# Performance work log

Hardware: AMD Instinct MI355X
Metric: run time of the kernel (lower is better)

Reference implementation:

```python
import jax, jax.numpy as jnp
import numpy as np

N_EMBED = 1024
NUM_EXPERTS = 8
TOP_K = 2
D_FF = 4 * N_EMBED
B, S = 4, 2048


def setup_inputs() -> dict:
    key = jax.random.key(0)
    ks = jax.random.split(key, 8)
    s = 0.02
    return {
        "x": jax.random.normal(ks[0], (B, S, N_EMBED), jnp.float32),
        "noise": jax.random.normal(ks[1], (B, S, NUM_EXPERTS), jnp.float32),
        "w_route": jax.random.normal(ks[2], (N_EMBED, NUM_EXPERTS), jnp.float32) * s,
        "b_route": jnp.zeros((NUM_EXPERTS,), jnp.float32),
        "w_noise": jax.random.normal(ks[3], (N_EMBED, NUM_EXPERTS), jnp.float32) * s,
        "b_noise": jnp.zeros((NUM_EXPERTS,), jnp.float32),
        "w1": jax.random.normal(ks[4], (NUM_EXPERTS, N_EMBED, D_FF), jnp.float32) * s,
        "b1": jnp.zeros((NUM_EXPERTS, D_FF), jnp.float32),
        "w2": jax.random.normal(ks[5], (NUM_EXPERTS, D_FF, N_EMBED), jnp.float32) * s,
        "b2": jnp.zeros((NUM_EXPERTS, N_EMBED), jnp.float32),
    }


def reference(x, noise, w_route, b_route, w_noise, b_noise, w1, b1, w2, b2):
    # NoisyTopkRouter: logits + N(0,1)*softplus(noise_logits), top-k, softmax
    # over a sparse (-inf filled) logit matrix -> gates are exactly 0 for
    # non-selected experts.
    logits = x @ w_route + b_route                                   # [B,S,E]
    noise_logits = x @ w_noise + b_noise                             # [B,S,E]
    noisy = logits + noise * jax.nn.softplus(noise_logits)           # [B,S,E]
    _, topi = jax.lax.top_k(noisy, TOP_K)                            # [B,S,k]
    sel = jax.nn.one_hot(topi, NUM_EXPERTS, dtype=bool).any(-2)      # [B,S,E]
    sparse_logits = jnp.where(sel, noisy, -jnp.inf)
    gates = jax.nn.softmax(sparse_logits, axis=-1)                   # [B,S,E]

    T = x.shape[0] * x.shape[1]
    xf = x.reshape(T, N_EMBED)                                       # [T,d]
    gf = gates.reshape(T, NUM_EXPERTS)                               # [T,E]

    # Dense per-expert MLP weighted by gates; gate==0 for unselected tokens,
    # so this matches the masked gather/scatter of the original exactly.
    out = jnp.zeros_like(xf)
    for e in range(NUM_EXPERTS):
        h = jax.nn.relu(xf @ w1[e] + b1[e])                          # [T,4d]
        y = h @ w2[e] + b2[e]                                        # [T,d]
        out = out + y * gf[:, e:e + 1]
    return out.reshape(x.shape)
```

## Files before the change

### kernel.cpp

```cpp
#include <hip/hip_runtime.h>

typedef __bf16 bf16_t;
typedef __bf16 bf16x8 __attribute__((ext_vector_type(8)));
typedef __bf16 bf16x4 __attribute__((ext_vector_type(4)));
typedef float  f32x4  __attribute__((ext_vector_type(4)));

#define T_TOK 8192
#define DIM   1024
#define DFF   4096
#define NEXP  8

__device__ __forceinline__ void gll16(const void* g, void* l) {
    __builtin_amdgcn_global_load_lds(
        (const __attribute__((address_space(1))) char*)g,
        (__attribute__((address_space(3))) char*)l, 16, 0, 0);
}

__global__ __launch_bounds__(256) void transpose_cvt_kernel(
    const float* __restrict__ src, bf16_t* __restrict__ dst, int R, int C) {
    __shared__ float t[64][65];
    int e = blockIdx.z;
    src += (size_t)e * R * C;
    dst += (size_t)e * R * C;
    int r0 = blockIdx.y * 64, c0 = blockIdx.x * 64;
    int tid = threadIdx.x;
    {
        int cg = tid & 15, r = tid >> 4;
#pragma unroll
        for (int i = 0; i < 4; ++i) {
            int rr = r + i * 16;
            float4 v = *(const float4*)&src[(size_t)(r0 + rr) * C + c0 + cg * 4];
            t[rr][cg * 4 + 0] = v.x; t[rr][cg * 4 + 1] = v.y;
            t[rr][cg * 4 + 2] = v.z; t[rr][cg * 4 + 3] = v.w;
        }
    }
    __syncthreads();
    {
        int rr = tid & 7, c = tid >> 3;
#pragma unroll
        for (int i = 0; i < 2; ++i) {
            int cc = c + i * 32;
            bf16x8 o;
#pragma unroll
            for (int j = 0; j < 8; ++j) o[j] = (bf16_t)t[rr * 8 + j][cc];
            *(bf16x8*)&dst[(size_t)(c0 + cc) * R + r0 + rr * 8] = o;
        }
    }
}

__global__ __launch_bounds__(256) void router_kernel(
    const float* __restrict__ x, const float* __restrict__ noise,
    const float* __restrict__ w_route, const float* __restrict__ b_route,
    const float* __restrict__ w_noise, const float* __restrict__ b_noise,
    int* __restrict__ counts, int* __restrict__ lists, float* __restrict__ gate_tok)
{
    int wave = threadIdx.x >> 6;
    int lane = threadIdx.x & 63;
    int t = blockIdx.x * 4 + wave;
    if (t >= T_TOK) return;

    const float* xr = x + (size_t)t * DIM;
    double aR[NEXP], aN[NEXP];
#pragma unroll
    for (int e = 0; e < NEXP; ++e) { aR[e] = 0.0; aN[e] = 0.0; }

#pragma unroll 4
    for (int i = 0; i < 16; ++i) {
        int k = lane + i * 64;
        double xv = (double)xr[k];
        const float4* wr4 = (const float4*)(w_route + (size_t)k * 8);
        const float4* wn4 = (const float4*)(w_noise + (size_t)k * 8);
        float4 r0 = wr4[0], r1 = wr4[1];
        float4 n0 = wn4[0], n1 = wn4[1];
        aR[0] += xv * (double)r0.x; aR[1] += xv * (double)r0.y;
        aR[2] += xv * (double)r0.z; aR[3] += xv * (double)r0.w;
        aR[4] += xv * (double)r1.x; aR[5] += xv * (double)r1.y;
        aR[6] += xv * (double)r1.z; aR[7] += xv * (double)r1.w;
        aN[0] += xv * (double)n0.x; aN[1] += xv * (double)n0.y;
        aN[2] += xv * (double)n0.z; aN[3] += xv * (double)n0.w;
        aN[4] += xv * (double)n1.x; aN[5] += xv * (double)n1.y;
        aN[6] += xv * (double)n1.z; aN[7] += xv * (double)n1.w;
    }
#pragma unroll
    for (int e = 0; e < NEXP; ++e) {
        for (int s = 1; s < 64; s <<= 1) {
            aR[e] += __shfl_xor(aR[e], s);
            aN[e] += __shfl_xor(aN[e], s);
        }
    }
    if (lane == 0) {
        double nv[NEXP];
#pragma unroll
        for (int e = 0; e < NEXP; ++e) {
            double lg = aR[e] + (double)b_route[e];
            double nl = aN[e] + (double)b_noise[e];
            double sp = (nl > 30.0) ? nl : log1p(exp(nl));
            nv[e] = lg + (double)noise[(size_t)t * 8 + e] * sp;
        }
        int i1 = 0;
#pragma unroll
        for (int e = 1; e < NEXP; ++e) if (nv[e] > nv[i1]) i1 = e;
        int i2 = (i1 == 0) ? 1 : 0;
#pragma unroll
        for (int e = 0; e < NEXP; ++e) if (e != i1 && nv[e] > nv[i2]) i2 = e;
        double m = nv[i1];
        double e2 = exp(nv[i2] - m);
        double s = 1.0 + e2;
        gate_tok[2 * t + 0] = (float)(1.0 / s);
        gate_tok[2 * t + 1] = (float)(e2 / s);
        int p1 = atomicAdd(&counts[i1], 1);
        lists[i1 * T_TOK + p1] = 2 * t + 0;
        int p2 = atomicAdd(&counts[i2], 1);
        lists[i2 * T_TOK + p2] = 2 * t + 1;
    }
}

__global__ void prefix_kernel(const int* __restrict__ counts, int* __restrict__ bases) {
    if (threadIdx.x == 0 && blockIdx.x == 0) {
        int s = 0;
#pragma unroll
        for (int e = 0; e < NEXP; ++e) { bases[e] = s; s += counts[e]; }
    }
}

__global__ __launch_bounds__(256) void pack_a_kernel(
    const float* __restrict__ x, const int* __restrict__ bases,
    const int* __restrict__ lists, bf16_t* __restrict__ Ap, int* __restrict__ inv)
{
    int wave = threadIdx.x >> 6, lane = threadIdx.x & 63;
    int p = blockIdx.x * 4 + wave;
    int e = 0;
#pragma unroll
    for (int i = 1; i < NEXP; ++i) e += (p >= bases[i]);
    int pos = p - bases[e];
    int entry = lists[e * T_TOK + pos];
    if (lane == 0) inv[entry] = p;
    const float4* src = (const float4*)(x + (size_t)(entry >> 1) * DIM);
    bf16x4* dst = (bf16x4*)(Ap + (size_t)p * DIM);
#pragma unroll
    for (int j = 0; j < 4; ++j) {
        float4 v = src[lane + j * 64];
        bf16x4 o;
        o[0] = (bf16_t)v.x; o[1] = (bf16_t)v.y; o[2] = (bf16_t)v.z; o[3] = (bf16_t)v.w;
        dst[lane + j * 64] = o;
    }
}

template<int K, int MODE>
__global__ __launch_bounds__(256) void moe_gemm_kernel(
    const bf16_t* __restrict__ Asrc, const bf16_t* __restrict__ Wt,
    const float* __restrict__ bias,
    const int* __restrict__ counts, const int* __restrict__ bases,
    const int* __restrict__ lists, const float* __restrict__ gate_tok,
    bf16_t* __restrict__ Hout, float* __restrict__ Yp)
{
    constexpr int N = (MODE == 0) ? DFF : DIM;
    constexpr int NT = K / 64;
    constexpr int NY = N / 128;

    int wg = blockIdx.x + 64 * (blockIdx.y + NY * blockIdx.z);
    int e = wg & 7;
    int inner = wg >> 3;
    int xi = inner & 63;
    int yi = inner >> 6;

    int cnt = counts[e];
    int m0 = xi * 128;
    if (m0 >= cnt) return;
    int base = bases[e];
    int n0 = yi * 128;
    const int* list = lists + e * T_TOK;
    const bf16_t* W = Wt + (size_t)e * N * K;

    __shared__ __attribute__((aligned(16))) bf16_t Ah0[128 * 64];
    __shared__ __attribute__((aligned(16))) bf16_t Bh0[128 * 64];
    __shared__ __attribute__((aligned(16))) bf16_t Ah1[128 * 64];
    __shared__ __attribute__((aligned(16))) bf16_t Bh1[128 * 64];

    int tid = threadIdx.x;
    int lane = tid & 63;
    int wave = tid >> 6;
    int wr = wave >> 1, wc = wave & 1;

    int kcs = (((lane & 7) ^ (lane >> 3)) << 3);
    const bf16_t* pA[4];
    const bf16_t* pB[4];
#pragma unroll
    for (int i = 0; i < 4; ++i) {
        int c = wave * 4 + i;
        int r = c * 8 + (lane >> 3);
        int ridx = m0 + r; if (ridx > cnt - 1) ridx = cnt - 1;
        pA[i] = Asrc + (size_t)(base + ridx) * K + kcs;
        pB[i] = W + (size_t)(n0 + r) * K + kcs;
    }

    f32x4 acc[4][4];
#pragma unroll
    for (int m = 0; m < 4; ++m)
#pragma unroll
        for (int n = 0; n < 4; ++n)
            acc[m][n] = (f32x4){0.f, 0.f, 0.f, 0.f};

    int g = lane >> 4, ln15 = lane & 15, ln7 = lane & 7;

#define STAGE(An, Bn, k0) do {                                               \
    _Pragma("unroll") for (int i = 0; i < 4; ++i) {                          \
        int c = wave * 4 + i;                                                \
        gll16(pA[i] + (k0), (An) + c * 512);                                 \
        gll16(pB[i] + (k0), (Bn) + c * 512);                                 \
    } } while (0)

#define COMPUTE(Ab, Bb) do {                                                 \
    _Pragma("unroll") for (int kk = 0; kk < 2; ++kk) {                       \
        bf16x8 a[4], b[4];                                                   \
        int sw = (((kk * 4 + g) ^ ln7) << 3);                                \
        _Pragma("unroll") for (int n = 0; n < 4; ++n)                        \
            b[n] = *(const bf16x8*)((Bb) + (wc * 64 + n * 16 + ln15) * 64 + sw); \
        _Pragma("unroll") for (int m = 0; m < 4; ++m)                        \
            a[m] = *(const bf16x8*)((Ab) + (wr * 64 + m * 16 + ln15) * 64 + sw); \
        __builtin_amdgcn_s_setprio(1);                                       \
        _Pragma("unroll") for (int m = 0; m < 4; ++m)                        \
            _Pragma("unroll") for (int n = 0; n < 4; ++n)                    \
                acc[m][n] = __builtin_amdgcn_mfma_f32_16x16x32_bf16(a[m], b[n], acc[m][n], 0, 0, 0); \
        __builtin_amdgcn_s_setprio(0);                                       \
    } } while (0)

#define FENCE() __builtin_amdgcn_sched_barrier(0)
#define WAITV(n) asm volatile("s_waitcnt vmcnt(" #n ")" ::: "memory")

    STAGE(Ah0, Bh0, 0);

    for (int kt = 0; kt < NT; kt += 2) {
        if (kt + 1 < NT) { STAGE(Ah1, Bh1, (kt + 1) * 64); WAITV(8); }
        else             { WAITV(0); }
        FENCE(); __builtin_amdgcn_s_barrier(); FENCE();
        COMPUTE(Ah0, Bh0);
        FENCE(); __builtin_amdgcn_s_barrier(); FENCE();
        if (kt + 2 < NT) { STAGE(Ah0, Bh0, (kt + 2) * 64); WAITV(8); }
        else             { WAITV(0); }
        FENCE(); __builtin_amdgcn_s_barrier(); FENCE();
        COMPUTE(Ah1, Bh1);
        FENCE(); __builtin_amdgcn_s_barrier(); FENCE();
    }
#undef STAGE
#undef COMPUTE
#undef FENCE
#undef WAITV

    int l4 = lane >> 4;
    float bs[4];
#pragma unroll
    for (int n = 0; n < 4; ++n)
        bs[n] = bias[e * N + n0 + wc * 64 + n * 16 + ln15];
#pragma unroll
    for (int m = 0; m < 4; ++m) {
#pragma unroll
        for (int j = 0; j < 4; ++j) {
            int grow = m0 + wr * 64 + m * 16 + l4 * 4 + j;
            if (grow >= cnt) continue;
            if constexpr (MODE == 0) {
#pragma unroll
                for (int n = 0; n < 4; ++n) {
                    int gcol = n0 + wc * 64 + n * 16 + ln15;
                    float v = acc[m][n][j] + bs[n];
                    Hout[(size_t)(base + grow) * DFF + gcol] = (bf16_t)fmaxf(v, 0.f);
                }
            } else {
                float gt = gate_tok[list[grow]];
#pragma unroll
                for (int n = 0; n < 4; ++n) {
                    int gcol = n0 + wc * 64 + n * 16 + ln15;
                    Yp[(size_t)(base + grow) * DIM + gcol] = gt * (acc[m][n][j] + bs[n]);
                }
            }
        }
    }
}

__global__ __launch_bounds__(256) void combine_kernel(
    const float* __restrict__ Yp, const int* __restrict__ inv,
    float* __restrict__ out)
{
#pragma unroll
    for (int q = 0; q < 2; ++q) {
        int t = blockIdx.x * 2 + q;
        int p0 = inv[2 * t], p1 = inv[2 * t + 1];
        const float4* a = (const float4*)(Yp + (size_t)p0 * DIM);
        const float4* b = (const float4*)(Yp + (size_t)p1 * DIM);
        float4* o = (float4*)(out + (size_t)t * DIM);
        int i = threadIdx.x;
        float4 va = a[i], vb = b[i];
        o[i] = make_float4(va.x + vb.x, va.y + vb.y, va.z + vb.z, va.w + vb.w);
    }
}

extern "C" void kernel_launch(void* const* d_in, const int* in_sizes, int n_in,
                              void* d_out, int out_size, void* d_ws, size_t ws_size,
                              hipStream_t stream) {
    const float* x       = (const float*)d_in[0];
    const float* noise   = (const float*)d_in[1];
    const float* w_route = (const float*)d_in[2];
    const float* b_route = (const float*)d_in[3];
    const float* w_noise = (const float*)d_in[4];
    const float* b_noise = (const float*)d_in[5];
    const float* w1      = (const float*)d_in[6];
    const float* b1      = (const float*)d_in[7];
    const float* w2      = (const float*)d_in[8];
    const float* b2      = (const float*)d_in[9];
    float* out = (float*)d_out;

    char* ws = (char*)d_ws;
    size_t off = 0;
    auto alloc = [&](size_t bytes) {
        off = (off + 255) & ~(size_t)255;
        size_t r = off; off += bytes; return r;
    };
    int*    counts   = (int*)   (ws + alloc(32));
    int*    bases    = (int*)   (ws + alloc(32));
    int*    lists    = (int*)   (ws + alloc((size_t)NEXP * T_TOK * 4));
    float*  gate_tok = (float*) (ws + alloc((size_t)T_TOK * 2 * 4));
    int*    inv      = (int*)   (ws + alloc((size_t)T_TOK * 2 * 4));
    bf16_t* w1t      = (bf16_t*)(ws + alloc((size_t)NEXP * DFF * DIM * 2));
    bf16_t* w2t      = (bf16_t*)(ws + alloc((size_t)NEXP * DIM * DFF * 2));
    bf16_t* Ap       = (bf16_t*)(ws + alloc((size_t)T_TOK * 2 * DIM * 2));
    bf16_t* H        = (bf16_t*)(ws + alloc((size_t)T_TOK * 2 * DFF * 2));
    float*  Yp       = (float*)w1t;
    (void)ws_size; (void)in_sizes; (void)n_in; (void)out_size;

    hipMemsetAsync(counts, 0, 32, stream);

    transpose_cvt_kernel<<<dim3(DFF / 64, DIM / 64, NEXP), 256, 0, stream>>>(w1, w1t, DIM, DFF);
    transpose_cvt_kernel<<<dim3(DIM / 64, DFF / 64, NEXP), 256, 0, stream>>>(w2, w2t, DFF, DIM);

    router_kernel<<<T_TOK / 4, 256, 0, stream>>>(x, noise, w_route, b_route, w_noise, b_noise,
                                                 counts, lists, gate_tok);
    prefix_kernel<<<1, 64, 0, stream>>>(counts, bases);
    pack_a_kernel<<<T_TOK * 2 / 4, 256, 0, stream>>>(x, bases, lists, Ap, inv);

    moe_gemm_kernel<DIM, 0><<<dim3(64, DFF / 128, NEXP), 256, 0, stream>>>(
        Ap, w1t, b1, counts, bases, lists, gate_tok, H, nullptr);
    moe_gemm_kernel<DFF, 1><<<dim3(64, DIM / 128, NEXP), 256, 0, stream>>>(
        H, w2t, b2, counts, bases, lists, gate_tok, nullptr, Yp);

    combine_kernel<<<T_TOK / 2, 256, 0, stream>>>(Yp, inv, out);
}
```

Measured before the change: 780.2 us.

## Enlarge MoE GEMM tile to 256x128 with K-step 32

Changes the grouped expert GEMM tile from 128x128 with a 64-wide K step to 256x128 with a 32-wide K step. Each wave now computes 128x64 outputs with 8x4 MFMA accumulators, which raises arithmetic intensity per LDS byte and per global load. The LDS swizzle, staging layout, wait counts and launch grid are reworked to match. In exchange it uses more accumulator registers, which may reduce occupancy. It also needs twice as many K iterations with barriers, and padding waste grows for experts whose token count is not a multiple of 256.

```diff
diff --git a/kernel.cpp b/kernel.cpp
--- a/kernel.cpp
+++ b/kernel.cpp
@@ -155,75 +155,79 @@
     bf16_t* __restrict__ Hout, float* __restrict__ Yp)
 {
     constexpr int N = (MODE == 0) ? DFF : DIM;
-    constexpr int NT = K / 64;
+    constexpr int NT = K / 32;
     constexpr int NY = N / 128;
 
-    int wg = blockIdx.x + 64 * (blockIdx.y + NY * blockIdx.z);
+    int wg = blockIdx.x + 32 * (blockIdx.y + NY * blockIdx.z);
     int e = wg & 7;
     int inner = wg >> 3;
-    int xi = inner & 63;
-    int yi = inner >> 6;
+    int xi = inner & 31;
+    int yi = inner >> 5;
 
     int cnt = counts[e];
-    int m0 = xi * 128;
+    int m0 = xi * 256;
     if (m0 >= cnt) return;
     int base = bases[e];
     int n0 = yi * 128;
     const int* list = lists + e * T_TOK;
     const bf16_t* W = Wt + (size_t)e * N * K;
 
-    __shared__ __attribute__((aligned(16))) bf16_t Ah0[128 * 64];
-    __shared__ __attribute__((aligned(16))) bf16_t Bh0[128 * 64];
-    __shared__ __attribute__((aligned(16))) bf16_t Ah1[128 * 64];
-    __shared__ __attribute__((aligned(16))) bf16_t Bh1[128 * 64];
+    __shared__ __attribute__((aligned(16))) bf16_t Ah0[256 * 32];
+    __shared__ __attribute__((aligned(16))) bf16_t Bh0[128 * 32];
+    __shared__ __attribute__((aligned(16))) bf16_t Ah1[256 * 32];
+    __shared__ __attribute__((aligned(16))) bf16_t Bh1[128 * 32];
 
     int tid = threadIdx.x;
     int lane = tid & 63;
     int wave = tid >> 6;
     int wr = wave >> 1, wc = wave & 1;
 
-    int kcs = (((lane & 7) ^ (lane >> 3)) << 3);
+    int kcs = (((lane & 3) ^ ((lane >> 3) & 3)) << 3);
     const bf16_t* pA[4];
-    const bf16_t* pB[4];
+    const bf16_t* pB[2];
 #pragma unroll
     for (int i = 0; i < 4; ++i) {
         int c = wave * 4 + i;
-        int r = c * 8 + (lane >> 3);
+        int r = c * 16 + (lane >> 2);
         int ridx = m0 + r; if (ridx > cnt - 1) ridx = cnt - 1;
         pA[i] = Asrc + (size_t)(base + ridx) * K + kcs;
+    }
+#pragma unroll
+    for (int i = 0; i < 2; ++i) {
+        int c = wave * 2 + i;
+        int r = c * 16 + (lane >> 2);
         pB[i] = W + (size_t)(n0 + r) * K + kcs;
     }
 
-    f32x4 acc[4][4];
-#pragma unroll
-    for (int m = 0; m < 4; ++m)
+    f32x4 acc[8][4];
+#pragma unroll
+    for (int m = 0; m < 8; ++m)
 #pragma unroll
         for (int n = 0; n < 4; ++n)
             acc[m][n] = (f32x4){0.f, 0.f, 0.f, 0.f};
 
-    int g = lane >> 4, ln15 = lane & 15, ln7 = lane & 7;
+    int g = lane >> 4, ln15 = lane & 15;
+    int sw = ((g ^ ((ln15 >> 1) & 3)) << 3);
 
 #define STAGE(An, Bn, k0) do {                                               \
-    _Pragma("unroll") for (int i = 0; i < 4; ++i) {                          \
-        int c = wave * 4 + i;                                                \
-        gll16(pA[i] + (k0), (An) + c * 512);                                 \
-        gll16(pB[i] + (k0), (Bn) + c * 512);                                 \
-    } } while (0)
+    _Pragma("unroll") for (int i = 0; i < 4; ++i)                            \
+        gll16(pA[i] + (k0), (An) + (wave * 4 + i) * 512);                    \
+    _Pragma("unroll") for (int i = 0; i < 2; ++i)                            \
+        gll16(pB[i] + (k0), (Bn) + (wave * 2 + i) * 512);                    \
+    } while (0)
 
 #define COMPUTE(Ab, Bb) do {                                                 \
-    _Pragma("unroll") for (int kk = 0; kk < 2; ++kk) {                       \
-        bf16x8 a[4], b[4];                                                   \
-        int sw = (((kk * 4 + g) ^ ln7) << 3);                                \
+    bf16x8 b[4];                                                             \
+    _Pragma("unroll") for (int n = 0; n < 4; ++n)                            \
+        b[n] = *(const bf16x8*)((Bb) + (wc * 64 + n * 16 + ln15) * 32 + sw); \
+    __builtin_amdgcn_s_setprio(1);                                           \
+    _Pragma("unroll") for (int m = 0; m < 8; ++m) {                          \
+        bf16x8 a = *(const bf16x8*)((Ab) + (wr * 128 + m * 16 + ln15) * 32 + sw); \
         _Pragma("unroll") for (int n = 0; n < 4; ++n)                        \
-            b[n] = *(const bf16x8*)((Bb) + (wc * 64 + n * 16 + ln15) * 64 + sw); \
-        _Pragma("unroll") for (int m = 0; m < 4; ++m)                        \
-            a[m] = *(const bf16x8*)((Ab) + (wr * 64 + m * 16 + ln15) * 64 + sw); \
-        __builtin_amdgcn_s_setprio(1);                                       \
-        _Pragma("unroll") for (int m = 0; m < 4; ++m)                        \
-            _Pragma("unroll") for (int n = 0; n < 4; ++n)                    \
-                acc[m][n] = __builtin_amdgcn_mfma_f32_16x16x32_bf16(a[m], b[n], acc[m][n], 0, 0, 0); \
-        __builtin_amdgcn_s_setprio(0);                                       \
-    } } while (0)
+            acc[m][n] = __builtin_amdgcn_mfma_f32_16x16x32_bf16(a, b[n], acc[m][n], 0, 0, 0); \
+    }                                                                        \
+    __builtin_amdgcn_s_setprio(0);                                           \
+    } while (0)
 
 #define FENCE() __builtin_amdgcn_sched_barrier(0)
 #define WAITV(n) asm volatile("s_waitcnt vmcnt(" #n ")" ::: "memory")
@@ -231,12 +235,12 @@
     STAGE(Ah0, Bh0, 0);
 
     for (int kt = 0; kt < NT; kt += 2) {
-        if (kt + 1 < NT) { STAGE(Ah1, Bh1, (kt + 1) * 64); WAITV(8); }
+        if (kt + 1 < NT) { STAGE(Ah1, Bh1, (kt + 1) * 32); WAITV(6); }
         else             { WAITV(0); }
         FENCE(); __builtin_amdgcn_s_barrier(); FENCE();
         COMPUTE(Ah0, Bh0);
         FENCE(); __builtin_amdgcn_s_barrier(); FENCE();
-        if (kt + 2 < NT) { STAGE(Ah0, Bh0, (kt + 2) * 64); WAITV(8); }
+        if (kt + 2 < NT) { STAGE(Ah0, Bh0, (kt + 2) * 32); WAITV(6); }
         else             { WAITV(0); }
         FENCE(); __builtin_amdgcn_s_barrier(); FENCE();
         COMPUTE(Ah1, Bh1);
@@ -253,10 +257,10 @@
     for (int n = 0; n < 4; ++n)
         bs[n] = bias[e * N + n0 + wc * 64 + n * 16 + ln15];
 #pragma unroll
-    for (int m = 0; m < 4; ++m) {
+    for (int m = 0; m < 8; ++m) {
 #pragma unroll
         for (int j = 0; j < 4; ++j) {
-            int grow = m0 + wr * 64 + m * 16 + l4 * 4 + j;
+            int grow = m0 + wr * 128 + m * 16 + l4 * 4 + j;
             if (grow >= cnt) continue;
             if constexpr (MODE == 0) {
 #pragma unroll
@@ -337,9 +341,9 @@
     prefix_kernel<<<1, 64, 0, stream>>>(counts, bases);
     pack_a_kernel<<<T_TOK * 2 / 4, 256, 0, stream>>>(x, bases, lists, Ap, inv);
 
-    moe_gemm_kernel<DIM, 0><<<dim3(64, DFF / 128, NEXP), 256, 0, stream>>>(
+    moe_gemm_kernel<DIM, 0><<<dim3(32, DFF / 128, NEXP), 256, 0, stream>>>(
         Ap, w1t, b1, counts, bases, lists, gate_tok, H, nullptr);
-    moe_gemm_kernel<DFF, 1><<<dim3(64, DIM / 128, NEXP), 256, 0, stream>>>(
+    moe_gemm_kernel<DFF, 1><<<dim3(32, DIM / 128, NEXP), 256, 0, stream>>>(
         H, w2t, b2, counts, bases, lists, gate_tok, nullptr, Yp);
 
     combine_kernel<<<T_TOK / 2, 256, 0, stream>>>(Yp, inv, out);
```

Result: slower. 1.025 ms (+31.4%).

## Inline expert prefix sums and restructure GEMM double-buffer to one barrier per tile

Applied to the files above, without the earlier changes.

The single-thread prefix_kernel launch is removed. pack_a and the MoE GEMM kernels now compute expert base offsets themselves from the 8 counts. The GEMM main loop changes from a stage, partial-wait, barrier, compute, barrier sequence to staging the next tile, computing the current one, then a full vmcnt drain and a single barrier. This halves the barriers per K-tile and removes one kernel launch. The cost is that each compute step now waits on the full drain of the prefetch, so less memory latency may be hidden if loads outlast compute.

```diff
diff --git a/kernel.cpp b/kernel.cpp
--- a/kernel.cpp
+++ b/kernel.cpp
@@ -115,24 +115,22 @@
     }
 }
 
-__global__ void prefix_kernel(const int* __restrict__ counts, int* __restrict__ bases) {
-    if (threadIdx.x == 0 && blockIdx.x == 0) {
-        int s = 0;
-#pragma unroll
-        for (int e = 0; e < NEXP; ++e) { bases[e] = s; s += counts[e]; }
-    }
-}
-
 __global__ __launch_bounds__(256) void pack_a_kernel(
-    const float* __restrict__ x, const int* __restrict__ bases,
+    const float* __restrict__ x, const int* __restrict__ counts,
     const int* __restrict__ lists, bf16_t* __restrict__ Ap, int* __restrict__ inv)
 {
     int wave = threadIdx.x >> 6, lane = threadIdx.x & 63;
     int p = blockIdx.x * 4 + wave;
+    int bs[NEXP];
+    {
+        int s = 0;
+#pragma unroll
+        for (int i = 0; i < NEXP; ++i) { bs[i] = s; s += counts[i]; }
+    }
     int e = 0;
 #pragma unroll
-    for (int i = 1; i < NEXP; ++i) e += (p >= bases[i]);
-    int pos = p - bases[e];
+    for (int i = 1; i < NEXP; ++i) e += (p >= bs[i]);
+    int pos = p - bs[e];
     int entry = lists[e * T_TOK + pos];
     if (lane == 0) inv[entry] = p;
     const float4* src = (const float4*)(x + (size_t)(entry >> 1) * DIM);
@@ -150,8 +148,8 @@
 __global__ __launch_bounds__(256) void moe_gemm_kernel(
     const bf16_t* __restrict__ Asrc, const bf16_t* __restrict__ Wt,
     const float* __restrict__ bias,
-    const int* __restrict__ counts, const int* __restrict__ bases,
-    const int* __restrict__ lists, const float* __restrict__ gate_tok,
+    const int* __restrict__ counts, const int* __restrict__ lists,
+    const float* __restrict__ gate_tok,
     bf16_t* __restrict__ Hout, float* __restrict__ Yp)
 {
     constexpr int N = (MODE == 0) ? DFF : DIM;
@@ -164,10 +162,19 @@
     int xi = inner & 63;
     int yi = inner >> 6;
 
-    int cnt = counts[e];
+    int cnt, base;
+    {
+        int s = 0, c = 0;
+#pragma unroll
+        for (int i = 0; i < NEXP; ++i) {
+            int ci = counts[i];
+            if (i == e) { base = s; c = ci; }
+            s += ci;
+        }
+        cnt = c;
+    }
     int m0 = xi * 128;
     if (m0 >= cnt) return;
-    int base = bases[e];
     int n0 = yi * 128;
     const int* list = lists + e * T_TOK;
     const bf16_t* W = Wt + (size_t)e * N * K;
@@ -226,26 +233,25 @@
     } } while (0)
 
 #define FENCE() __builtin_amdgcn_sched_barrier(0)
-#define WAITV(n) asm volatile("s_waitcnt vmcnt(" #n ")" ::: "memory")
+#define DRAIN() asm volatile("s_waitcnt vmcnt(0)" ::: "memory")
+#define BARR()  do { FENCE(); __builtin_amdgcn_s_barrier(); FENCE(); } while (0)
 
     STAGE(Ah0, Bh0, 0);
+    DRAIN(); BARR();
 
     for (int kt = 0; kt < NT; kt += 2) {
-        if (kt + 1 < NT) { STAGE(Ah1, Bh1, (kt + 1) * 64); WAITV(8); }
-        else             { WAITV(0); }
-        FENCE(); __builtin_amdgcn_s_barrier(); FENCE();
+        if (kt + 1 < NT) STAGE(Ah1, Bh1, (kt + 1) * 64);
         COMPUTE(Ah0, Bh0);
-        FENCE(); __builtin_amdgcn_s_barrier(); FENCE();
-        if (kt + 2 < NT) { STAGE(Ah0, Bh0, (kt + 2) * 64); WAITV(8); }
-        else             { WAITV(0); }
-        FENCE(); __builtin_amdgcn_s_barrier(); FENCE();
+        DRAIN(); BARR();
+        if (kt + 2 < NT) STAGE(Ah0, Bh0, (kt + 2) * 64);
         COMPUTE(Ah1, Bh1);
-        FENCE(); __builtin_amdgcn_s_barrier(); FENCE();
+        DRAIN(); BARR();
     }
 #undef STAGE
 #undef COMPUTE
 #undef FENCE
-#undef WAITV
+#undef DRAIN
+#undef BARR
 
     int l4 = lane >> 4;
     float bs[4];
@@ -316,7 +322,6 @@
         size_t r = off; off += bytes; return r;
     };
     int*    counts   = (int*)   (ws + alloc(32));
-    int*    bases    = (int*)   (ws + alloc(32));
     int*    lists    = (int*)   (ws + alloc((size_t)NEXP * T_TOK * 4));
     float*  gate_tok = (float*) (ws + alloc((size_t)T_TOK * 2 * 4));
     int*    inv      = (int*)   (ws + alloc((size_t)T_TOK * 2 * 4));
@@ -334,13 +339,12 @@
 
     router_kernel<<<T_TOK / 4, 256, 0, stream>>>(x, noise, w_route, b_route, w_noise, b_noise,
                                                  counts, lists, gate_tok);
-    prefix_kernel<<<1, 64, 0, stream>>>(counts, bases);
-    pack_a_kernel<<<T_TOK * 2 / 4, 256, 0, stream>>>(x, bases, lists, Ap, inv);
+    pack_a_kernel<<<T_TOK * 2 / 4, 256, 0, stream>>>(x, counts, lists, Ap, inv);
 
     moe_gemm_kernel<DIM, 0><<<dim3(64, DFF / 128, NEXP), 256, 0, stream>>>(
-        Ap, w1t, b1, counts, bases, lists, gate_tok, H, nullptr);
+        Ap, w1t, b1, counts, lists, gate_tok, H, nullptr);
     moe_gemm_kernel<DFF, 1><<<dim3(64, DIM / 128, NEXP), 256, 0, stream>>>(
-        H, w2t, b2, counts, bases, lists, gate_tok, nullptr, Yp);
+        H, w2t, b2, counts, lists, gate_tok, nullptr, Yp);
 
     combine_kernel<<<T_TOK / 2, 256, 0, stream>>>(Yp, inv, out);
 }
```

After: 816.7 us. 1.05x slower.

## Merge weight transposes with counter reset and store expert outputs in bf16

Applied to the files above, without the earlier changes.

Combines the two weight transpose/convert launches and the counts memset into one kernel, removing two launches. Expert output partials Yp are now written and read as bf16 instead of fp32, halving the traffic of the second GEMM epilogue and of the combine kernel. The cost is lower precision in the per-expert partial outputs before they are summed.

```diff
diff --git a/kernel.cpp b/kernel.cpp
--- a/kernel.cpp
+++ b/kernel.cpp
@@ -16,14 +16,10 @@
         (__attribute__((address_space(3))) char*)l, 16, 0, 0);
 }
 
-__global__ __launch_bounds__(256) void transpose_cvt_kernel(
-    const float* __restrict__ src, bf16_t* __restrict__ dst, int R, int C) {
-    __shared__ float t[64][65];
-    int e = blockIdx.z;
-    src += (size_t)e * R * C;
-    dst += (size_t)e * R * C;
-    int r0 = blockIdx.y * 64, c0 = blockIdx.x * 64;
-    int tid = threadIdx.x;
+__device__ __forceinline__ void transpose_tile(
+    const float* __restrict__ src, bf16_t* __restrict__ dst,
+    int R, int C, int r0, int c0, int tid, float (*t)[65])
+{
     {
         int cg = tid & 15, r = tid >> 4;
 #pragma unroll
@@ -45,6 +41,29 @@
             for (int j = 0; j < 8; ++j) o[j] = (bf16_t)t[rr * 8 + j][cc];
             *(bf16x8*)&dst[(size_t)(c0 + cc) * R + r0 + rr * 8] = o;
         }
+    }
+}
+
+__global__ __launch_bounds__(256) void transpose_both_kernel(
+    const float* __restrict__ w1, const float* __restrict__ w2,
+    bf16_t* __restrict__ w1t, bf16_t* __restrict__ w2t,
+    int* __restrict__ counts)
+{
+    __shared__ float t[64][65];
+    int id = blockIdx.x;
+    int tid = threadIdx.x;
+    if (id == 0 && tid < NEXP) counts[tid] = 0;
+    if (id < 8192) {
+        int e = id >> 10, rem = id & 1023;
+        int bx = rem & 63, by = rem >> 6;
+        transpose_tile(w1 + (size_t)e * DIM * DFF, w1t + (size_t)e * DIM * DFF,
+                       DIM, DFF, by * 64, bx * 64, tid, t);
+    } else {
+        int id2 = id - 8192;
+        int e = id2 >> 10, rem = id2 & 1023;
+        int bx = rem & 15, by = rem >> 4;
+        transpose_tile(w2 + (size_t)e * DFF * DIM, w2t + (size_t)e * DFF * DIM,
+                       DFF, DIM, by * 64, bx * 64, tid, t);
     }
 }
 
@@ -152,7 +171,7 @@
     const float* __restrict__ bias,
     const int* __restrict__ counts, const int* __restrict__ bases,
     const int* __restrict__ lists, const float* __restrict__ gate_tok,
-    bf16_t* __restrict__ Hout, float* __restrict__ Yp)
+    bf16_t* __restrict__ Hout, bf16_t* __restrict__ Yp)
 {
     constexpr int N = (MODE == 0) ? DFF : DIM;
     constexpr int NT = K / 64;
@@ -270,7 +289,7 @@
 #pragma unroll
                 for (int n = 0; n < 4; ++n) {
                     int gcol = n0 + wc * 64 + n * 16 + ln15;
-                    Yp[(size_t)(base + grow) * DIM + gcol] = gt * (acc[m][n][j] + bs[n]);
+                    Yp[(size_t)(base + grow) * DIM + gcol] = (bf16_t)(gt * (acc[m][n][j] + bs[n]));
                 }
             }
         }
@@ -278,19 +297,20 @@
 }
 
 __global__ __launch_bounds__(256) void combine_kernel(
-    const float* __restrict__ Yp, const int* __restrict__ inv,
+    const bf16_t* __restrict__ Yp, const int* __restrict__ inv,
     float* __restrict__ out)
 {
 #pragma unroll
     for (int q = 0; q < 2; ++q) {
         int t = blockIdx.x * 2 + q;
         int p0 = inv[2 * t], p1 = inv[2 * t + 1];
-        const float4* a = (const float4*)(Yp + (size_t)p0 * DIM);
-        const float4* b = (const float4*)(Yp + (size_t)p1 * DIM);
+        const bf16x4* a = (const bf16x4*)(Yp + (size_t)p0 * DIM);
+        const bf16x4* b = (const bf16x4*)(Yp + (size_t)p1 * DIM);
         float4* o = (float4*)(out + (size_t)t * DIM);
         int i = threadIdx.x;
-        float4 va = a[i], vb = b[i];
-        o[i] = make_float4(va.x + vb.x, va.y + vb.y, va.z + vb.z, va.w + vb.w);
+        bf16x4 va = a[i], vb = b[i];
+        o[i] = make_float4((float)va[0] + (float)vb[0], (float)va[1] + (float)vb[1],
+                           (float)va[2] + (float)vb[2], (float)va[3] + (float)vb[3]);
     }
 }
 
@@ -324,13 +344,10 @@
     bf16_t* w2t      = (bf16_t*)(ws + alloc((size_t)NEXP * DIM * DFF * 2));
     bf16_t* Ap       = (bf16_t*)(ws + alloc((size_t)T_TOK * 2 * DIM * 2));
     bf16_t* H        = (bf16_t*)(ws + alloc((size_t)T_TOK * 2 * DFF * 2));
-    float*  Yp       = (float*)w1t;
+    bf16_t* Yp       = w1t;
     (void)ws_size; (void)in_sizes; (void)n_in; (void)out_size;
 
-    hipMemsetAsync(counts, 0, 32, stream);
-
-    transpose_cvt_kernel<<<dim3(DFF / 64, DIM / 64, NEXP), 256, 0, stream>>>(w1, w1t, DIM, DFF);
-    transpose_cvt_kernel<<<dim3(DIM / 64, DFF / 64, NEXP), 256, 0, stream>>>(w2, w2t, DFF, DIM);
+    transpose_both_kernel<<<16384, 256, 0, stream>>>(w1, w2, w1t, w2t, counts);
 
     router_kernel<<<T_TOK / 4, 256, 0, stream>>>(x, noise, w_route, b_route, w_noise, b_noise,
                                                  counts, lists, gate_tok);
```

Result: faster. 763.8 us (-2.1%).
